# Performance work log

Hardware: AMD Instinct MI355X
Metric: run time of the kernel (lower is better)

## Reference

```python
import jax, jax.numpy as jnp
import numpy as np

B = 2000           # number of events (segments)
N = 1_000_000      # total points (sum of num_points)
D_IN, H, D_OUT = 16, 256, 128
EPS = 1e-5


def _layer_norm(x, g, b):
    m = x.mean(-1, keepdims=True)
    v = x.var(-1, keepdims=True)
    return (x - m) * jax.lax.rsqrt(v + EPS) * g + b


def setup_inputs() -> dict:
    key = jax.random.key(0)
    ks = jax.random.split(key, 8)
    # ragged counts, all positive, summing exactly to N
    rng = np.random.default_rng(0)
    counts = np.full(B, N // B, dtype=np.int64)
    d = rng.integers(-400, 401, size=B // 2)
    counts[: B // 2] += d
    counts[B // 2 :] -= d
    assert counts.sum() == N and (counts > 0).all()
    z_t = jax.random.normal(ks[0], (N, D_IN), dtype=jnp.float32)
    def lin(k, fi, fo):
        return jax.random.normal(k, (fi, fo), dtype=jnp.float32) / np.sqrt(fi)
    return {
        "z_t": z_t,
        "W1": lin(ks[1], D_IN, H), "b1": jnp.zeros((H,), jnp.float32),
        "g1": jnp.ones((H,), jnp.float32), "be1": jnp.zeros((H,), jnp.float32),
        "W2": lin(ks[2], H, H), "b2": jnp.zeros((H,), jnp.float32),
        "g2": jnp.ones((H,), jnp.float32), "be2": jnp.zeros((H,), jnp.float32),
        "W3": lin(ks[3], H, D_OUT), "b3": jnp.zeros((D_OUT,), jnp.float32),
        "num_points": jnp.asarray(counts, dtype=jnp.int64),
    }


def reference(z_t, W1, b1, g1, be1, W2, b2, g2, be2, W3, b3, num_points):
    # per-point phi MLP: Linear -> LN -> ReLU (x2) -> Linear
    h = jax.nn.relu(_layer_norm(z_t @ W1 + b1, g1, be1))
    h = jax.nn.relu(_layer_norm(h @ W2 + b2, g2, be2))
    phi = h @ W3 + b3                                  # [N, D_OUT]
    # fused ragged mean-pool + broadcast back (replaces split/stack/repeat_interleave)
    seg = jnp.repeat(jnp.arange(B), num_points, total_repeat_length=N)  # [N]
    sums = jax.ops.segment_sum(phi, seg, num_segments=B)                # [B, D_OUT]
    emb = sums / num_points[:, None].astype(phi.dtype)                  # mean pooling
    return emb[seg]                                                     # [N, D_OUT]
```

## Files before the change

### kernel.cpp

```cpp
#include <hip/hip_runtime.h>
#include <hip/hip_bf16.h>
#include <cstdint>
#include <cstddef>

#define NPTS  1000000
#define BSEG  2000
#define DIN   16
#define HDIM  256
#define DOUT  128
#define NTILE (NPTS / 32)
#define NWG   512

typedef __bf16          bf16x8 __attribute__((ext_vector_type(8)));
typedef unsigned short  us16x8 __attribute__((ext_vector_type(8)));
typedef unsigned int    u32x4  __attribute__((ext_vector_type(4)));
typedef float           f32x4  __attribute__((ext_vector_type(4)));

static __device__ __forceinline__ unsigned short f2bf(float x) {
    unsigned int u = __float_as_uint(x);
    u += 0x7fffu + ((u >> 16) & 1u);
    return (unsigned short)(u >> 16);
}

static __device__ __forceinline__ bf16x8 ldb8(const unsigned short* p) {
    u32x4 v = *(const u32x4*)p;
    return __builtin_bit_cast(bf16x8, v);
}
static __device__ __forceinline__ f32x4 mfma16(bf16x8 a, bf16x8 b, f32x4 c) {
    return __builtin_amdgcn_mfma_f32_16x16x32_bf16(a, b, c, 0, 0, 0);
}
static __device__ __forceinline__ void keep(bf16x8& v) {
    u32x4 u = __builtin_bit_cast(u32x4, v);
    unsigned a0 = u[0], a1 = u[1], a2 = u[2], a3 = u[3];
    asm volatile("" : "+v"(a0), "+v"(a1), "+v"(a2), "+v"(a3));
    u32x4 r; r[0] = a0; r[1] = a1; r[2] = a2; r[3] = a3;
    v = __builtin_bit_cast(bf16x8, r);
}

__global__ __launch_bounds__(1024) void scan_counts(const int* __restrict__ counts,
                                                    int* __restrict__ offsets) {
    __shared__ int a[2048];
    const int t = threadIdx.x;
    a[t]        = (t        < BSEG) ? counts[t]        : 0;
    a[t + 1024] = (t + 1024 < BSEG) ? counts[t + 1024] : 0;
    for (int s = 1; s < 2048; s <<= 1) {
        __syncthreads();
        int x1 = (t >= s) ? a[t - s] : 0;
        int x2 = a[t + 1024 - s];
        __syncthreads();
        a[t] += x1;
        a[t + 1024] += x2;
    }
    __syncthreads();
    if (t == 0) offsets[0] = 0;
    offsets[t + 1] = a[t];
    if (t + 1024 < BSEG) offsets[t + 1025] = a[t + 1024];
}

__global__ __launch_bounds__(256) void fill_seg(const int* __restrict__ offsets,
                                                unsigned short* __restrict__ seg) {
    const int b  = blockIdx.x;
    const int lo = offsets[b], hi = offsets[b + 1];
    for (int i = lo + threadIdx.x; i < hi; i += 256) seg[i] = (unsigned short)b;
}

__global__ __launch_bounds__(256) void prep_weights(const float* __restrict__ W1,
                                                    const float* __restrict__ W2,
                                                    unsigned short* __restrict__ w1t,
                                                    unsigned short* __restrict__ w2t) {
    const int i = blockIdx.x * 256 + threadIdx.x;
    if (i < HDIM * 32) {
        int n = i >> 5, k = i & 31;
        w1t[i] = (k < DIN) ? f2bf(W1[k * HDIM + n]) : (unsigned short)0;
    } else {
        int j = i - HDIM * 32;
        if (j < HDIM * HDIM) {
            int n = j >> 8, k = j & 255;
            w2t[j] = f2bf(W2[k * HDIM + n]);
        }
    }
}

__global__ __launch_bounds__(256, 2) void fused_phi_pool(
    const float* __restrict__ z,
    const unsigned short* __restrict__ w1t,
    const unsigned short* __restrict__ w2t,
    const float* __restrict__ b1, const float* __restrict__ g1, const float* __restrict__ be1,
    const float* __restrict__ b2, const float* __restrict__ g2, const float* __restrict__ be2,
    const unsigned short* __restrict__ seg,
    float* __restrict__ sums_h) {
    __shared__ __align__(16) unsigned short h1[32][264];
    __shared__ __align__(16) float part[2][32][8];
    __shared__ __align__(16) int seg_sm[2][32];

    const int tid  = threadIdx.x;
    const int wave = tid >> 6;
    const int lane = tid & 63;
    const int l15  = lane & 15;
    const int quad = lane >> 4;
    const int colw = wave * 64 + l15;

    bf16x8 bw1[4];
    bf16x8 bw2[4][8];
#pragma unroll
    for (int t = 0; t < 4; ++t) {
        const int n = (wave * 4 + t) * 16 + l15;
        bw1[t] = ldb8(w1t + n * 32 + quad * 8);
        keep(bw1[t]);
#pragma unroll
        for (int ks = 0; ks < 8; ++ks) {
            bw2[t][ks] = ldb8(w2t + n * 256 + ks * 32 + quad * 8);
            keep(bw2[t][ks]);
        }
    }
    float b1v[4], g1v[4], e1v[4], b2v[4], g2v[4], e2v[4];
#pragma unroll
    for (int t = 0; t < 4; ++t) {
        const int c = colw + t * 16;
        b1v[t] = b1[c]; g1v[t] = g1[c]; e1v[t] = be1[c];
        b2v[t] = b2[c]; g2v[t] = g2[c]; e2v[t] = be2[c];
    }

    int p = 0;
    for (int tile = blockIdx.x; tile < NTILE; tile += NWG, p ^= 1) {
        const int base = tile * 32;
        if (tid < 32) seg_sm[p][tid] = (int)seg[base + tid];

        f32x4 a1[2][4];
#pragma unroll
        for (int mb = 0; mb < 2; ++mb) {
            bf16x8 af;
            if (quad < 2) {
                const float* zp = z + (size_t)(base + mb * 16 + l15) * DIN + quad * 8;
                float4 v0 = *(const float4*)zp;
                float4 v1 = *(const float4*)(zp + 4);
                us16x8 u;
                u[0] = f2bf(v0.x); u[1] = f2bf(v0.y); u[2] = f2bf(v0.z); u[3] = f2bf(v0.w);
                u[4] = f2bf(v1.x); u[5] = f2bf(v1.y); u[6] = f2bf(v1.z); u[7] = f2bf(v1.w);
                af = __builtin_bit_cast(bf16x8, u);
            } else {
                us16x8 u = {0, 0, 0, 0, 0, 0, 0, 0};
                af = __builtin_bit_cast(bf16x8, u);
            }
            const f32x4 zero = {0.f, 0.f, 0.f, 0.f};
#pragma unroll
            for (int t = 0; t < 4; ++t) a1[mb][t] = mfma16(af, bw1[t], zero);
        }
#pragma unroll
        for (int mb = 0; mb < 2; ++mb) {
            float s[4], q[4];
#pragma unroll
            for (int r = 0; r < 4; ++r) {
                float sv = 0.f, qv = 0.f;
#pragma unroll
                for (int t = 0; t < 4; ++t) {
                    float y = a1[mb][t][r] + b1v[t];
                    a1[mb][t][r] = y;
                    sv += y; qv += y * y;
                }
                s[r] = sv; q[r] = qv;
            }
#pragma unroll
            for (int m = 1; m <= 8; m <<= 1) {
#pragma unroll
                for (int r = 0; r < 4; ++r) {
                    s[r] += __shfl_xor(s[r], m, 64);
                    q[r] += __shfl_xor(q[r], m, 64);
                }
            }
            if (l15 == 0) {
#pragma unroll
                for (int r = 0; r < 4; ++r)
                    *(float2*)&part[p][mb * 16 + quad * 4 + r][wave * 2] =
                        make_float2(s[r], q[r]);
            }
        }
        __syncthreads();
#pragma unroll
        for (int mb = 0; mb < 2; ++mb) {
#pragma unroll
            for (int r = 0; r < 4; ++r) {
                const int row = mb * 16 + quad * 4 + r;
                float4 pa = *(const float4*)&part[p][row][0];
                float4 pb = *(const float4*)&part[p][row][4];
                float st = pa.x + pa.z + pb.x + pb.z;
                float qt = pa.y + pa.w + pb.y + pb.w;
                float mean = st * (1.f / 256.f);
                float var  = qt * (1.f / 256.f) - mean * mean;
                float rs   = rsqrtf(fmaxf(var, 0.f) + 1e-5f);
#pragma unroll
                for (int t = 0; t < 4; ++t) {
                    float A = rs * g1v[t];
                    float y = fmaxf(fmaf(a1[mb][t][r], A, fmaf(-mean, A, e1v[t])), 0.f);
                    h1[row][colw + t * 16] = f2bf(y);
                }
            }
        }
        __syncthreads();

        f32x4 a2[2][4];
#pragma unroll
        for (int mb = 0; mb < 2; ++mb) {
            const f32x4 zero = {0.f, 0.f, 0.f, 0.f};
#pragma unroll
            for (int t = 0; t < 4; ++t) a2[mb][t] = zero;
#pragma unroll
            for (int ks = 0; ks < 8; ++ks) {
                bf16x8 af = ldb8(&h1[mb * 16 + l15][ks * 32 + quad * 8]);
#pragma unroll
                for (int t = 0; t < 4; ++t) a2[mb][t] = mfma16(af, bw2[t][ks], a2[mb][t]);
            }
        }
#pragma unroll
        for (int mb = 0; mb < 2; ++mb) {
            float s[4], q[4];
#pragma unroll
            for (int r = 0; r < 4; ++r) {
                float sv = 0.f, qv = 0.f;
#pragma unroll
                for (int t = 0; t < 4; ++t) {
                    float y = a2[mb][t][r] + b2v[t];
                    a2[mb][t][r] = y;
                    sv += y; qv += y * y;
                }
                s[r] = sv; q[r] = qv;
            }
#pragma unroll
            for (int m = 1; m <= 8; m <<= 1) {
#pragma unroll
                for (int r = 0; r < 4; ++r) {
                    s[r] += __shfl_xor(s[r], m, 64);
                    q[r] += __shfl_xor(q[r], m, 64);
                }
            }
            if (l15 == 0) {
#pragma unroll
                for (int r = 0; r < 4; ++r)
                    *(float2*)&part[p][mb * 16 + quad * 4 + r][wave * 2] =
                        make_float2(s[r], q[r]);
            }
        }
        __syncthreads();
#pragma unroll
        for (int mb = 0; mb < 2; ++mb) {
#pragma unroll
            for (int r = 0; r < 4; ++r) {
                const int row = mb * 16 + quad * 4 + r;
                float4 pa = *(const float4*)&part[p][row][0];
                float4 pb = *(const float4*)&part[p][row][4];
                float st = pa.x + pa.z + pb.x + pb.z;
                float qt = pa.y + pa.w + pb.y + pb.w;
                float mean = st * (1.f / 256.f);
                float var  = qt * (1.f / 256.f) - mean * mean;
                float rs   = rsqrtf(fmaxf(var, 0.f) + 1e-5f);
#pragma unroll
                for (int t = 0; t < 4; ++t) {
                    float A = rs * g2v[t];
                    a2[mb][t][r] =
                        fmaxf(fmaf(a2[mb][t][r], A, fmaf(-mean, A, e2v[t])), 0.f);
                }
            }
        }

        const int s0  = seg_sm[p][0];
        const int s31 = seg_sm[p][31];
        if (s0 == s31) {
#pragma unroll
            for (int t = 0; t < 4; ++t) {
                float cs = a2[0][t][0] + a2[0][t][1] + a2[0][t][2] + a2[0][t][3]
                         + a2[1][t][0] + a2[1][t][1] + a2[1][t][2] + a2[1][t][3];
                cs += __shfl_xor(cs, 16, 64);
                cs += __shfl_xor(cs, 32, 64);
                if (quad == 0)
                    atomicAdd(&sums_h[s0 * HDIM + colw + t * 16], cs);
            }
        } else {
            const int* sgp = &seg_sm[p][0];
            float m0[4], m1[4];
#pragma unroll
            for (int r = 0; r < 4; ++r) {
                m0[r] = (sgp[quad * 4 + r]      == s0) ? 1.f : 0.f;
                m1[r] = (sgp[16 + quad * 4 + r] == s0) ? 1.f : 0.f;
            }
#pragma unroll
            for (int t = 0; t < 4; ++t) {
                float cs = 0.f, ca = 0.f;
#pragma unroll
                for (int r = 0; r < 4; ++r) {
                    cs += a2[0][t][r] + a2[1][t][r];
                    ca = fmaf(a2[0][t][r], m0[r], ca);
                    ca = fmaf(a2[1][t][r], m1[r], ca);
                }
                cs += __shfl_xor(cs, 16, 64);
                cs += __shfl_xor(cs, 32, 64);
                ca += __shfl_xor(ca, 16, 64);
                ca += __shfl_xor(ca, 32, 64);
                if (quad == 0) {
                    atomicAdd(&sums_h[s0  * HDIM + colw + t * 16], ca);
                    atomicAdd(&sums_h[s31 * HDIM + colw + t * 16], cs - ca);
                }
            }
        }
    }
}

__global__ __launch_bounds__(256) void emb_gemm(const float* __restrict__ sums_h,
                                                const float* __restrict__ W3,
                                                const float* __restrict__ b3,
                                                const int* __restrict__ counts,
                                                float* __restrict__ emb) {
    const int b = blockIdx.x * 2 + (threadIdx.x >> 7);
    const int o = threadIdx.x & 127;
    const float* sh = sums_h + b * HDIM;
    float acc = 0.f;
#pragma unroll 8
    for (int k = 0; k < HDIM; ++k) acc = fmaf(sh[k], W3[k * DOUT + o], acc);
    emb[b * DOUT + o] = acc / (float)counts[b] + b3[o];
}

__global__ __launch_bounds__(256) void broadcast_out(const float* __restrict__ emb,
                                                     const unsigned short* __restrict__ seg,
                                                     float* __restrict__ out) {
    const int idx = blockIdx.x * 256 + threadIdx.x;
    const int n = idx >> 5, qd = idx & 31;
    const int s = seg[n];
    ((float4*)out)[idx] = ((const float4*)emb)[s * 32 + qd];
}

extern "C" void kernel_launch(void* const* d_in, const int* in_sizes, int n_in,
                              void* d_out, int out_size, void* d_ws, size_t ws_size,
                              hipStream_t stream) {
    const float* z   = (const float*)d_in[0];
    const float* W1  = (const float*)d_in[1];
    const float* b1  = (const float*)d_in[2];
    const float* g1  = (const float*)d_in[3];
    const float* be1 = (const float*)d_in[4];
    const float* W2  = (const float*)d_in[5];
    const float* b2  = (const float*)d_in[6];
    const float* g2  = (const float*)d_in[7];
    const float* be2 = (const float*)d_in[8];
    const float* W3  = (const float*)d_in[9];
    const float* b3  = (const float*)d_in[10];
    const int* counts = (const int*)d_in[11];
    float* out = (float*)d_out;

    char* ws = (char*)d_ws;
    float*          sums_h  = (float*)(ws);
    float*          emb     = (float*)(ws + 2048000);
    int*            offsets = (int*)  (ws + 3072000);
    unsigned short* seg     = (unsigned short*)(ws + 3080016);
    unsigned short* w1t     = (unsigned short*)(ws + 5080016);
    unsigned short* w2t     = (unsigned short*)(ws + 5096400);

    hipMemsetAsync(sums_h, 0, (size_t)BSEG * HDIM * sizeof(float), stream);
    scan_counts<<<1, 1024, 0, stream>>>(counts, offsets);
    fill_seg<<<BSEG, 256, 0, stream>>>(offsets, seg);
    prep_weights<<<(HDIM * 32 + HDIM * HDIM) / 256, 256, 0, stream>>>(W1, W2, w1t, w2t);
    fused_phi_pool<<<NWG, 256, 0, stream>>>(z, w1t, w2t,
                                            b1, g1, be1, b2, g2, be2,
                                            seg, sums_h);
    emb_gemm<<<BSEG / 2, 256, 0, stream>>>(sums_h, W3, b3, counts, emb);
    broadcast_out<<<NPTS * 32 / 256, 256, 0, stream>>>(emb, seg, out);
}
```

Before: 1.068 ms.

## Prefetch next z tile, use DPP row reductions, widen broadcast stores

The fused MLP kernel now loads the next tile's z rows into registers one iteration ahead, hiding global load latency behind the current tile's MFMA work. The LayerNorm row sums over 16 lanes use DPP row_shr-style updates instead of shfl_xor, which avoids LDS-permute traffic. The broadcast kernel writes two float4 per thread with half as many threads. Together these add register pressure under the 2-waves launch bound, and the DPP pattern must produce the full 16-lane total that lane l15==0 reads.

```diff
diff --git a/kernel.cpp b/kernel.cpp
--- a/kernel.cpp
+++ b/kernel.cpp
@@ -35,6 +35,18 @@
     asm volatile("" : "+v"(a0), "+v"(a1), "+v"(a2), "+v"(a3));
     u32x4 r; r[0] = a0; r[1] = a1; r[2] = a2; r[3] = a3;
     v = __builtin_bit_cast(bf16x8, r);
+}
+
+static __device__ __forceinline__ float rsum16(float x) {
+    x += __builtin_bit_cast(float, __builtin_amdgcn_update_dpp(
+             0, __builtin_bit_cast(int, x), 0x128, 0xf, 0xf, false));
+    x += __builtin_bit_cast(float, __builtin_amdgcn_update_dpp(
+             0, __builtin_bit_cast(int, x), 0x124, 0xf, 0xf, false));
+    x += __builtin_bit_cast(float, __builtin_amdgcn_update_dpp(
+             0, __builtin_bit_cast(int, x), 0x122, 0xf, 0xf, false));
+    x += __builtin_bit_cast(float, __builtin_amdgcn_update_dpp(
+             0, __builtin_bit_cast(int, x), 0x121, 0xf, 0xf, false));
+    return x;
 }
 
 __global__ __launch_bounds__(1024) void scan_counts(const int* __restrict__ counts,
@@ -99,6 +111,7 @@
     const int l15  = lane & 15;
     const int quad = lane >> 4;
     const int colw = wave * 64 + l15;
+    const bool zlane = (quad < 2);
 
     bf16x8 bw1[4];
     bf16x8 bw2[4][8];
@@ -121,22 +134,48 @@
         b2v[t] = b2[c]; g2v[t] = g2[c]; e2v[t] = be2[c];
     }
 
+    float4 zn[2][2];
+    {
+        const int base0 = blockIdx.x * 32;
+        if (zlane) {
+#pragma unroll
+            for (int mb = 0; mb < 2; ++mb) {
+                const float* zp = z + (size_t)(base0 + mb * 16 + l15) * DIN + quad * 8;
+                zn[mb][0] = *(const float4*)zp;
+                zn[mb][1] = *(const float4*)(zp + 4);
+            }
+        }
+    }
+
     int p = 0;
     for (int tile = blockIdx.x; tile < NTILE; tile += NWG, p ^= 1) {
         const int base = tile * 32;
         if (tid < 32) seg_sm[p][tid] = (int)seg[base + tid];
 
+        float4 zc[2][2];
+#pragma unroll
+        for (int mb = 0; mb < 2; ++mb) { zc[mb][0] = zn[mb][0]; zc[mb][1] = zn[mb][1]; }
+        const int ntile = tile + NWG;
+        if (zlane && ntile < NTILE) {
+            const int nb = ntile * 32;
+#pragma unroll
+            for (int mb = 0; mb < 2; ++mb) {
+                const float* zp = z + (size_t)(nb + mb * 16 + l15) * DIN + quad * 8;
+                zn[mb][0] = *(const float4*)zp;
+                zn[mb][1] = *(const float4*)(zp + 4);
+            }
+        }
+
         f32x4 a1[2][4];
 #pragma unroll
         for (int mb = 0; mb < 2; ++mb) {
             bf16x8 af;
-            if (quad < 2) {
-                const float* zp = z + (size_t)(base + mb * 16 + l15) * DIN + quad * 8;
-                float4 v0 = *(const float4*)zp;
-                float4 v1 = *(const float4*)(zp + 4);
+            if (zlane) {
                 us16x8 u;
-                u[0] = f2bf(v0.x); u[1] = f2bf(v0.y); u[2] = f2bf(v0.z); u[3] = f2bf(v0.w);
-                u[4] = f2bf(v1.x); u[5] = f2bf(v1.y); u[6] = f2bf(v1.z); u[7] = f2bf(v1.w);
+                u[0] = f2bf(zc[mb][0].x); u[1] = f2bf(zc[mb][0].y);
+                u[2] = f2bf(zc[mb][0].z); u[3] = f2bf(zc[mb][0].w);
+                u[4] = f2bf(zc[mb][1].x); u[5] = f2bf(zc[mb][1].y);
+                u[6] = f2bf(zc[mb][1].z); u[7] = f2bf(zc[mb][1].w);
                 af = __builtin_bit_cast(bf16x8, u);
             } else {
                 us16x8 u = {0, 0, 0, 0, 0, 0, 0, 0};
@@ -158,15 +197,7 @@
                     a1[mb][t][r] = y;
                     sv += y; qv += y * y;
                 }
-                s[r] = sv; q[r] = qv;
-            }
-#pragma unroll
-            for (int m = 1; m <= 8; m <<= 1) {
-#pragma unroll
-                for (int r = 0; r < 4; ++r) {
-                    s[r] += __shfl_xor(s[r], m, 64);
-                    q[r] += __shfl_xor(q[r], m, 64);
-                }
+                s[r] = rsum16(sv); q[r] = rsum16(qv);
             }
             if (l15 == 0) {
 #pragma unroll
@@ -223,15 +254,7 @@
                     a2[mb][t][r] = y;
                     sv += y; qv += y * y;
                 }
-                s[r] = sv; q[r] = qv;
-            }
-#pragma unroll
-            for (int m = 1; m <= 8; m <<= 1) {
-#pragma unroll
-                for (int r = 0; r < 4; ++r) {
-                    s[r] += __shfl_xor(s[r], m, 64);
-                    q[r] += __shfl_xor(q[r], m, 64);
-                }
+                s[r] = rsum16(sv); q[r] = rsum16(qv);
             }
             if (l15 == 0) {
 #pragma unroll
@@ -322,9 +345,12 @@
                                                      const unsigned short* __restrict__ seg,
                                                      float* __restrict__ out) {
     const int idx = blockIdx.x * 256 + threadIdx.x;
-    const int n = idx >> 5, qd = idx & 31;
+    const int n = idx >> 4, oct = idx & 15;
     const int s = seg[n];
-    ((float4*)out)[idx] = ((const float4*)emb)[s * 32 + qd];
+    float4 v0 = ((const float4*)emb)[s * 32 + oct * 2];
+    float4 v1 = ((const float4*)emb)[s * 32 + oct * 2 + 1];
+    ((float4*)out)[idx * 2]     = v0;
+    ((float4*)out)[idx * 2 + 1] = v1;
 }
 
 extern "C" void kernel_launch(void* const* d_in, const int* in_sizes, int n_in,
@@ -360,5 +386,5 @@
                                             b1, g1, be1, b2, g2, be2,
                                             seg, sums_h);
     emb_gemm<<<BSEG / 2, 256, 0, stream>>>(sums_h, W3, b3, counts, emb);
-    broadcast_out<<<NPTS * 32 / 256, 256, 0, stream>>>(emb, seg, out);
-}
+    broadcast_out<<<NPTS * 16 / 256, 256, 0, stream>>>(emb, seg, out);
+}
```

After: 1.032 ms. 1.04x faster.
